# Kernel optimization log

Hardware: AMD Instinct MI355X
Metric: run time of the kernel (lower is better)

The kernel has to match this reference:

```python
import jax, jax.numpy as jnp
import numpy as np

NUM_EMBEDDINGS = 8192
EMBED_DIM = 256
BETA = 0.25  # commitment loss weight (self.beta in the torch module)


def setup_inputs() -> dict:
    key = jax.random.key(0)
    k1, k2 = jax.random.split(key)
    z = jax.random.normal(k1, (16, EMBED_DIM, 32, 32), dtype=jnp.float32)
    # learned codebook (nn.Embedding weight), default init ~ N(0,1); scale for realism
    codebook = jax.random.normal(k2, (NUM_EMBEDDINGS, EMBED_DIM), dtype=jnp.float32)
    return {"z": z, "codebook": codebook}


def reference(z, codebook):
    # channel_last: [B, C, H, W] -> [B, H, W, C]
    zl = jnp.transpose(z, (0, 2, 3, 1))
    # d = ||e||^2 - 2 z.e  (the ||z||^2 term is constant w.r.t. argmin, as in source)
    d = jnp.sum(codebook * codebook, axis=1) - 2.0 * jnp.einsum('bhwd,nd->bhwn', zl, codebook)
    index = jnp.argmin(d, axis=-1)          # [B, H, W] int
    z_q = codebook[index]                   # [B, H, W, C]
    loss = (jnp.mean((jax.lax.stop_gradient(z_q) - zl) ** 2)
            + BETA * jnp.mean((z_q - jax.lax.stop_gradient(zl)) ** 2))
    # straight-through estimator
    z_q_st = zl + jax.lax.stop_gradient(z_q - zl)
    # diversity: mean over batch of (#unique codes used per sample) / (#positions per sample)
    B = index.shape[0]
    flat = index.reshape(B, -1)             # [B, HW]
    presence = jnp.zeros((B, NUM_EMBEDDINGS), jnp.float32).at[
        jnp.arange(B)[:, None], flat].set(1.0)
    diversity = presence.sum() / jnp.float32(flat.size)
    # channel_first: [B, H, W, C] -> [B, C, H, W]
    z_q_out = jnp.transpose(z_q_st, (0, 3, 1, 2))
    return z_q_out, index, loss, diversity
```

## Files before the change

### kernel.cpp

```cpp
#include <hip/hip_runtime.h>
#include <cstdint>

typedef unsigned short u16;
typedef unsigned int   u32;
typedef __attribute__((ext_vector_type(8))) short bf16x8;
typedef __attribute__((ext_vector_type(4))) float f32x4;

#define NPOS    16384
#define DIM     256
#define NCODES  8192
#define ZSTRIDE 262144
#define NELEM   4194304
#define TAU     6e-3f
#define RCH     32


#define WS_AHI    0u
#define WS_ALO    8388608u
#define WS_BHI    16777216u
#define WS_BLO    20971520u
#define WS_E2     25165824u
#define WS_WV1    25198592u
#define WS_WI1    27295744u
#define WS_WV2    29392896u
#define WS_IDX    31490048u
#define WS_PRES   31555584u
#define WS_RCNT   31571968u
#define WS_LDEL   31571972u
#define WS_RLIST  31572224u
#define WS_PART   31637760u
#define WS_RBV    31638784u
#define WS_RBI    33735936u

__device__ __forceinline__ u16 f2bf(float x) {
    u32 u = __float_as_uint(x);
    return (u16)((u + 0x7FFFu + ((u >> 16) & 1u)) >> 16);
}
__device__ __forceinline__ float bf2f(u16 h) { return __uint_as_float((u32)h << 16); }

__device__ __forceinline__ void gload_lds16(const void* g, void* l) {
    __builtin_amdgcn_global_load_lds(
        (const __attribute__((address_space(1))) void*)g,
        (__attribute__((address_space(3))) void*)l, 16, 0, 0);
}

__device__ __forceinline__ void top2_push(float& v1, int& i1, float& v2, float d, int c) {
    const bool better = d < v1;
    v2 = fminf(v2, fmaxf(d, v1));
    v1 = fminf(v1, d);
    if (better) i1 = c;
}
__device__ __forceinline__ void top2_merge(float& v1, int& i1, float& v2,
                                           float ov1, int oi1, float ov2) {
    const bool better = ov1 < v1;
    v2 = fminf(fminf(v2, ov2), fmaxf(v1, ov1));
    v1 = fminf(v1, ov1);
    if (better) i1 = oi1;
}

__global__ __launch_bounds__(256)
void preprocess(const float* __restrict__ cb, const float* __restrict__ z,
                u16* __restrict__ Bhi, u16* __restrict__ Blo,
                u16* __restrict__ Ahi, u16* __restrict__ Alo,
                float* __restrict__ e2, u32* __restrict__ presence,
                int* __restrict__ rcnt, float* __restrict__ ldel) {
    __shared__ u16 his[128 * 34], los[128 * 34];
    const int bid = blockIdx.x;
    const int t   = threadIdx.x;

    if (bid < 2048) {
        if (bid < 16) presence[bid * 256 + t] = 0u;
        if (bid == 16 && t == 0) { rcnt[0] = 0; ldel[0] = 0.0f; }

        const int row  = bid * 4 + (t >> 6);
        const int lane = t & 63;
        const float4 v = *(const float4*)(cb + (size_t)row * DIM + lane * 4);
        float s = v.x * v.x + v.y * v.y + v.z * v.z + v.w * v.w;
#pragma unroll
        for (int o = 32; o > 0; o >>= 1) s += __shfl_xor(s, o);
        if (lane == 0) e2[row] = s;

        const float vv[4] = {v.x, v.y, v.z, v.w};
        u16 h[4], l[4];
#pragma unroll
        for (int j = 0; j < 4; ++j) { h[j] = f2bf(vv[j]); l[j] = f2bf(vv[j] - bf2f(h[j])); }

        const int nt = row >> 8, pr = row & 255, kt = lane >> 3;
        const int q  = (lane & 7) >> 1, off = (lane & 1) * 4;
        const int sw = (pr >> 1) & 3;
        const size_t dst = ((size_t)(nt * 8 + kt) * 256 + pr) * 32 + ((q ^ sw) << 3) + off;
        *(uint2*)(Bhi + dst) = make_uint2((u32)h[0] | ((u32)h[1] << 16), (u32)h[2] | ((u32)h[3] << 16));
        *(uint2*)(Blo + dst) = make_uint2((u32)l[0] | ((u32)l[1] << 16), (u32)l[2] | ((u32)l[3] << 16));
        return;
    }

    const int zb = bid - 2048;
    const int m128 = zb >> 3, kt = zb & 7;
    const int mtb = m128 >> 1, prb = (m128 & 1) * 128;
    const int b = m128 >> 3, hw0 = (m128 & 7) * 128;
    const int p = t & 127, ch = t >> 7;

#pragma unroll
    for (int sub = 0; sub < 16; ++sub) {
        const int cl = sub * 2 + ch;
        const float v = z[(size_t)b * ZSTRIDE + (size_t)(kt * 32 + cl) * 1024 + hw0 + p];
        const u16 h = f2bf(v);
        his[p * 34 + cl] = h;
        los[p * 34 + cl] = f2bf(v - bf2f(h));
    }
    __syncthreads();
    const int p2 = t >> 1, c0 = (t & 1) * 2;
    const int sw = (p2 >> 1) & 3;
    const size_t base = ((size_t)(mtb * 8 + kt) * 256 + prb + p2) * 32;
    u32 wh[8], wl[8];
    const int half = c0 * 8;
#pragma unroll
    for (int j = 0; j < 8; ++j) {
        wh[j] = (u32)his[p2 * 34 + half + 2 * j] | ((u32)his[p2 * 34 + half + 2 * j + 1] << 16);
        wl[j] = (u32)los[p2 * 34 + half + 2 * j] | ((u32)los[p2 * 34 + half + 2 * j + 1] << 16);
    }
    *(uint4*)(Ahi + base + (((c0 + 0) ^ sw) << 3)) = make_uint4(wh[0], wh[1], wh[2], wh[3]);
    *(uint4*)(Ahi + base + (((c0 + 1) ^ sw) << 3)) = make_uint4(wh[4], wh[5], wh[6], wh[7]);
    *(uint4*)(Alo + base + (((c0 + 0) ^ sw) << 3)) = make_uint4(wl[0], wl[1], wl[2], wl[3]);
    *(uint4*)(Alo + base + (((c0 + 1) ^ sw) << 3)) = make_uint4(wl[4], wl[5], wl[6], wl[7]);
}

__global__ __launch_bounds__(512, 2)
void gemm256(const u16* __restrict__ Ahi, const u16* __restrict__ Alo,
             const u16* __restrict__ Bhi, const u16* __restrict__ Blo,
             const float* __restrict__ e2,
             float* __restrict__ wv1, int* __restrict__ wi1, float* __restrict__ wv2) {
    __shared__ u16 sbuf[2][4][8192];
    __shared__ __align__(16) float e2s[1024];
    __shared__ float lv1[1024]; __shared__ int li1[1024]; __shared__ float lv2[1024];

    const int bid = blockIdx.x;
    const int ng  = bid & 7;
    const int mtb = bid >> 3;

    const int tid  = threadIdx.x;
    const int lane = tid & 63;
    const int wave = tid >> 6;
    const int wr   = wave >> 2, wc = wave & 3;
    const int l15  = lane & 15, lq = lane >> 4;
    const int woff = wave * 1024;
    const int src  = tid * 8;
    const int sel  = (l15 >> 1) & 3;
    const int ka   = ((lq ^ sel) << 3);

#define FRAG(base, row) (*(const bf16x8*)((base) + (row) * 32 + ka))
#define STAGE(bq, ss_) do {                                                     \
        const int ntl_ = (ss_) >> 3, kt_ = (ss_) & 7;                           \
        const int nt_  = ng * 4 + ntl_;                                         \
        const u16* Ah_ = Ahi + (size_t)(mtb * 8 + kt_) * 8192;                  \
        const u16* Al_ = Alo + (size_t)(mtb * 8 + kt_) * 8192;                  \
        const u16* Bh_ = Bhi + (size_t)(nt_ * 8 + kt_) * 8192;                  \
        const u16* Bl_ = Blo + (size_t)(nt_ * 8 + kt_) * 8192;                  \
        gload_lds16(Ah_ + src,        (char*)&sbuf[bq][0][0] + woff);           \
        gload_lds16(Ah_ + 4096 + src, (char*)&sbuf[bq][0][0] + 8192 + woff);    \
        gload_lds16(Al_ + src,        (char*)&sbuf[bq][1][0] + woff);           \
        gload_lds16(Al_ + 4096 + src, (char*)&sbuf[bq][1][0] + 8192 + woff);    \
        gload_lds16(Bh_ + src,        (char*)&sbuf[bq][2][0] + woff);           \
        gload_lds16(Bh_ + 4096 + src, (char*)&sbuf[bq][2][0] + 8192 + woff);    \
        gload_lds16(Bl_ + src,        (char*)&sbuf[bq][3][0] + woff);           \
        gload_lds16(Bl_ + 4096 + src, (char*)&sbuf[bq][3][0] + 8192 + woff);    \
    } while (0)

    f32x4 acc[8][4] = {};
    float e2v[4];
    int cbase = 0;

    e2s[tid]       = e2[ng * 1024 + tid];
    e2s[tid + 512] = e2[ng * 1024 + 512 + tid];
    __syncthreads();
    STAGE(0, 0);
    __syncthreads();

    for (int ss = 0; ss < 32; ++ss) {
        const int cur = ss & 1;
        if (ss < 31) STAGE(cur ^ 1, ss + 1);

        if ((ss & 7) == 0) {
            const int ntl = ss >> 3;
            cbase = (ng * 4 + ntl) * 256 + wc * 64 + l15;
            const int eb = ntl * 256 + wc * 64 + l15;
#pragma unroll
            for (int ni = 0; ni < 4; ++ni) e2v[ni] = e2s[eb + ni * 16];
        }

        const u16* Ah = &sbuf[cur][0][0];
        const u16* Al = &sbuf[cur][1][0];
        const u16* Bh = &sbuf[cur][2][0];
        const u16* Bl = &sbuf[cur][3][0];

        bf16x8 ah[8], bh[4], xx[8];
#pragma unroll
        for (int i = 0; i < 8; ++i) ah[i] = FRAG(Ah, wr * 128 + i * 16 + l15);
#pragma unroll
        for (int i = 0; i < 4; ++i) bh[i] = FRAG(Bh, wc * 64 + i * 16 + l15);
#pragma unroll
        for (int i = 0; i < 8; ++i)
#pragma unroll
            for (int j = 0; j < 4; ++j)
                acc[i][j] = __builtin_amdgcn_mfma_f32_16x16x32_bf16(ah[i], bh[j], acc[i][j], 0, 0, 0);
#pragma unroll
        for (int j = 0; j < 4; ++j) xx[j] = FRAG(Bl, wc * 64 + j * 16 + l15);
#pragma unroll
        for (int i = 0; i < 8; ++i)
#pragma unroll
            for (int j = 0; j < 4; ++j)
                acc[i][j] = __builtin_amdgcn_mfma_f32_16x16x32_bf16(ah[i], xx[j], acc[i][j], 0, 0, 0);
#pragma unroll
        for (int i = 0; i < 8; ++i) xx[i] = FRAG(Al, wr * 128 + i * 16 + l15);
#pragma unroll
        for (int i = 0; i < 8; ++i)
#pragma unroll
            for (int j = 0; j < 4; ++j)
                acc[i][j] = __builtin_amdgcn_mfma_f32_16x16x32_bf16(xx[i], bh[j], acc[i][j], 0, 0, 0);

        if ((ss & 7) == 7) {
            const int ntl = ss >> 3;
#pragma unroll
            for (int mi = 0; mi < 8; ++mi)
#pragma unroll
                for (int j = 0; j < 4; ++j) {
                    float v1 = 3e38f, v2 = 3e38f; int i1 = 0;
#pragma unroll
                    for (int ni = 0; ni < 4; ++ni) {
                        const float d = fmaf(-2.0f, acc[mi][ni][j], e2v[ni]);
                        top2_push(v1, i1, v2, d, cbase + ni * 16);
                    }
#pragma unroll
                    for (int off = 1; off <= 8; off <<= 1) {
                        const float ov1 = __shfl_xor(v1, off);
                        const int   oi1 = __shfl_xor(i1, off);
                        const float ov2 = __shfl_xor(v2, off);
                        top2_merge(v1, i1, v2, ov1, oi1, ov2);
                    }
                    if (l15 == 0) {
                        const int row = wr * 128 + mi * 16 + lq * 4 + j;
                        lv1[row * 4 + wc] = v1; li1[row * 4 + wc] = i1; lv2[row * 4 + wc] = v2;
                    }
                }
            __syncthreads();
            if (tid < 256) {
                float v1 = lv1[tid * 4], v2 = lv2[tid * 4]; int i1 = li1[tid * 4];
#pragma unroll
                for (int g = 1; g < 4; ++g)
                    top2_merge(v1, i1, v2, lv1[tid * 4 + g], li1[tid * 4 + g], lv2[tid * 4 + g]);
                const size_t o = (size_t)(ng * 4 + ntl) * NPOS + (size_t)mtb * 256 + tid;
                wv1[o] = v1; wi1[o] = i1; wv2[o] = v2;
            }
#pragma unroll
            for (int mi = 0; mi < 8; ++mi)
#pragma unroll
                for (int ni = 0; ni < 4; ++ni)
                    acc[mi][ni] = f32x4{0.f, 0.f, 0.f, 0.f};
        }
        __syncthreads();
    }
#undef FRAG
#undef STAGE
}

__global__ __launch_bounds__(256)
void merge_output(const float* __restrict__ wv1, const int* __restrict__ wi1,
                  const float* __restrict__ wv2,
                  const float* __restrict__ z, const float* __restrict__ cb,
                  float* __restrict__ out, float* __restrict__ out_idxf,
                  float* __restrict__ partial, u32* __restrict__ presence,
                  int* __restrict__ rcnt, int* __restrict__ rlist,
                  int* __restrict__ ws_idx) {
    __shared__ int codes[64];
    __shared__ float red[256];
    const int tile = blockIdx.x;
    const int b    = tile >> 4;
    const int hw0  = (tile & 15) * 64;
    const int tid  = threadIdx.x;
    const int m    = tid & 63;
    const int cg   = tid >> 6;

    if (cg == 0) {
        const int pos = tile * 64 + m;
        float v1 = 3e38f, v2 = 3e38f; int i1 = 0;
#pragma unroll
        for (int g = 0; g < 32; ++g) {
            const size_t o = (size_t)g * NPOS + pos;
            top2_merge(v1, i1, v2, wv1[o], wi1[o], wv2[o]);
        }
        codes[m]      = i1;
        ws_idx[pos]   = i1;
        out_idxf[pos] = (float)i1;
        if (v2 - v1 < TAU) {
            const int s = atomicAdd(rcnt, 1);
            rlist[s] = pos;
        } else {
            atomicOr(&presence[b * 256 + (i1 >> 5)], 1u << (i1 & 31));
        }
    }
    __syncthreads();

    const int code = codes[m];
    const float* crow = cb  + (size_t)code * DIM;
    const float* zb   = z   + (size_t)b * ZSTRIDE + hw0 + m;
    float*       ob   = out + (size_t)b * ZSTRIDE + hw0 + m;

    float lsum = 0.0f;
#pragma unroll
    for (int q = 0; q < 16; ++q) {
        const int c = (cg * 16 + q) * 4;
        const float4 e = *(const float4*)(crow + c);
        const float z0 = zb[(size_t)(c + 0) * 1024];
        const float z1 = zb[(size_t)(c + 1) * 1024];
        const float z2 = zb[(size_t)(c + 2) * 1024];
        const float z3 = zb[(size_t)(c + 3) * 1024];
        const float d0 = e.x - z0, d1 = e.y - z1, d2 = e.z - z2, d3 = e.w - z3;
        lsum += d0 * d0 + d1 * d1 + d2 * d2 + d3 * d3;
        ob[(size_t)(c + 0) * 1024] = z0 + d0;
        ob[(size_t)(c + 1) * 1024] = z1 + d1;
        ob[(size_t)(c + 2) * 1024] = z2 + d2;
        ob[(size_t)(c + 3) * 1024] = z3 + d3;
    }
    red[tid] = lsum;
    __syncthreads();
    for (int o = 128; o > 0; o >>= 1) {
        if (tid < o) red[tid] += red[tid + o];
        __syncthreads();
    }
    if (tid == 0) partial[tile] = red[0];
}

__global__ __launch_bounds__(256)
void rescue_scan(const float* __restrict__ z, const float* __restrict__ cb,
                 const float* __restrict__ e2, const int* __restrict__ rcnt,
                 const int* __restrict__ rlist,
                 float* __restrict__ rbv, int* __restrict__ rbi) {
    __shared__ float zvec[256];
    const int n = rcnt[0];
    const int t = threadIdx.x;
    const int w = t >> 6, l = t & 63;
    const int njobs = n * 8;
    for (int idx = blockIdx.x; idx < njobs; idx += gridDim.x) {
        const int e  = idx >> 3;
        const int cg = idx & 7;
        const int pos = rlist[e];
        const int b = pos >> 10, hw = pos & 1023;
        __syncthreads();
        zvec[t] = z[(size_t)b * ZSTRIDE + (size_t)t * 1024 + hw];
        __syncthreads();

        const int ch = cg * 4 + w;
        const int c0 = ch * 256 + l * 4;
        float bv = 3e38f; int bi = 0x7fffffff;
#pragma unroll
        for (int j = 0; j < 4; ++j) {
            const int c = c0 + j;
            const float* cr = cb + (size_t)c * DIM;
            float a0 = 0.f, a1 = 0.f, a2 = 0.f, a3 = 0.f;
#pragma unroll
            for (int k = 0; k < DIM; k += 16) {
                const float4 v0 = *(const float4*)(cr + k);
                const float4 v1 = *(const float4*)(cr + k + 4);
                const float4 v2 = *(const float4*)(cr + k + 8);
                const float4 v3 = *(const float4*)(cr + k + 12);
                a0 = fmaf(zvec[k + 0], v0.x, a0); a0 = fmaf(zvec[k + 1], v0.y, a0);
                a0 = fmaf(zvec[k + 2], v0.z, a0); a0 = fmaf(zvec[k + 3], v0.w, a0);
                a1 = fmaf(zvec[k + 4], v1.x, a1); a1 = fmaf(zvec[k + 5], v1.y, a1);
                a1 = fmaf(zvec[k + 6], v1.z, a1); a1 = fmaf(zvec[k + 7], v1.w, a1);
                a2 = fmaf(zvec[k + 8], v2.x, a2); a2 = fmaf(zvec[k + 9], v2.y, a2);
                a2 = fmaf(zvec[k +10], v2.z, a2); a2 = fmaf(zvec[k +11], v2.w, a2);
                a3 = fmaf(zvec[k +12], v3.x, a3); a3 = fmaf(zvec[k +13], v3.y, a3);
                a3 = fmaf(zvec[k +14], v3.z, a3); a3 = fmaf(zvec[k +15], v3.w, a3);
            }
            const float dot = (a0 + a1) + (a2 + a3);
            const float d = fmaf(-2.f, dot, e2[c]);
            if (d < bv) { bv = d; bi = c; }
        }
#pragma unroll
        for (int off = 1; off <= 32; off <<= 1) {
            const float ov = __shfl_xor(bv, off);
            const int   oi = __shfl_xor(bi, off);
            if (ov < bv || (ov == bv && oi < bi)) { bv = ov; bi = oi; }
        }
        if (l == 0) { rbv[e * RCH + ch] = bv; rbi[e * RCH + ch] = bi; }
    }
}

__global__ __launch_bounds__(256)
void rescue_fix(const float* __restrict__ z, const float* __restrict__ cb,
                const int* __restrict__ rcnt, const int* __restrict__ rlist,
                const float* __restrict__ rbv, const int* __restrict__ rbi,
                const int* __restrict__ ws_idx,
                float* __restrict__ out_idxf, u32* __restrict__ presence,
                float* __restrict__ out, float* __restrict__ ldel) {
    __shared__ int   bestc_sh;
    __shared__ float red[4];
    const int n = rcnt[0];
    const int t = threadIdx.x;
    for (int e = blockIdx.x; e < n; e += gridDim.x) {
        const int pos = rlist[e];
        const int b = pos >> 10, hw = pos & 1023;
        if (t < 64) {
            float v = 3e38f; int i = 0x7fffffff;
            if (t < 32) { v = rbv[e * RCH + t]; i = rbi[e * RCH + t]; }
#pragma unroll
            for (int off = 1; off <= 32; off <<= 1) {
                const float ov = __shfl_xor(v, off);
                const int   oi = __shfl_xor(i, off);
                if (ov < v || (ov == v && oi < i)) { v = ov; i = oi; }
            }
            if (t == 0) {
                bestc_sh = i;
                out_idxf[pos] = (float)i;
                atomicOr(&presence[b * 256 + (i >> 5)], 1u << (i & 31));
            }
        }
        __syncthreads();
        const int best = bestc_sh;
        const int old  = ws_idx[pos];
        if (best != old) {
            const float zv = z[(size_t)b * ZSTRIDE + (size_t)t * 1024 + hw];
            const float en = cb[(size_t)best * DIM + t];
            const float eo = cb[(size_t)old  * DIM + t];
            const float dn = en - zv, dold = eo - zv;
            out[(size_t)b * ZSTRIDE + (size_t)t * 1024 + hw] = zv + dn;
            float dl = dn * dn - dold * dold;
#pragma unroll
            for (int o = 32; o > 0; o >>= 1) dl += __shfl_xor(dl, o);
            if ((t & 63) == 0) red[t >> 6] = dl;
            __syncthreads();
            if (t == 0) atomicAdd(ldel, red[0] + red[1] + red[2] + red[3]);
        }
        __syncthreads();
    }
}

__global__ __launch_bounds__(256)
void finalize_kernel(const float* __restrict__ partial,
                     const u32* __restrict__ presence,
                     const float* __restrict__ ldel,
                     float* __restrict__ out_loss, float* __restrict__ out_div) {
    __shared__ float sred[256];
    __shared__ int   ired[256];
    const int tid = threadIdx.x;
    float s = partial[tid];
    int cnt = 0;
    for (int w = tid; w < 16 * 256; w += 256) cnt += __popc(presence[w]);
    sred[tid] = s; ired[tid] = cnt;
    __syncthreads();
    for (int o = 128; o > 0; o >>= 1) {
        if (tid < o) { sred[tid] += sred[tid + o]; ired[tid] += ired[tid + o]; }
        __syncthreads();
    }
    if (tid == 0) {
        out_loss[0] = 1.25f * (sred[0] + ldel[0]) / (float)NELEM;
        out_div[0]  = (float)ired[0] / (float)NPOS;
    }
}

extern "C" void kernel_launch(void* const* d_in, const int* in_sizes, int n_in,
                              void* d_out, int out_size, void* d_ws, size_t ws_size,
                              hipStream_t stream) {
    const float* z  = (const float*)d_in[0];
    const float* cb = (const float*)d_in[1];
    float* out = (float*)d_out;
    char*  ws  = (char*)d_ws;

    u16*   Ahi = (u16*)(ws + WS_AHI);
    u16*   Alo = (u16*)(ws + WS_ALO);
    u16*   Bhi = (u16*)(ws + WS_BHI);
    u16*   Blo = (u16*)(ws + WS_BLO);
    float* e2  = (float*)(ws + WS_E2);
    float* wv1 = (float*)(ws + WS_WV1);
    int*   wi1 = (int*)(ws + WS_WI1);
    float* wv2 = (float*)(ws + WS_WV2);
    int*   ws_idx = (int*)(ws + WS_IDX);
    u32*   presence = (u32*)(ws + WS_PRES);
    int*   rcnt  = (int*)(ws + WS_RCNT);
    float* ldel  = (float*)(ws + WS_LDEL);
    int*   rlist = (int*)(ws + WS_RLIST);
    float* partial = (float*)(ws + WS_PART);
    float* rbv = (float*)(ws + WS_RBV);
    int*   rbi = (int*)(ws + WS_RBI);

    float* out_zq   = out;
    float* out_idxf = out + NELEM;
    float* out_loss = out + NELEM + NPOS;
    float* out_div  = out + NELEM + NPOS + 1;

    preprocess<<<3072, 256, 0, stream>>>(cb, z, Bhi, Blo, Ahi, Alo, e2, presence, rcnt, ldel);
    gemm256<<<512, 512, 0, stream>>>(Ahi, Alo, Bhi, Blo, e2, wv1, wi1, wv2);
    merge_output<<<NPOS / 64, 256, 0, stream>>>(wv1, wi1, wv2, z, cb, out_zq, out_idxf,
                                                partial, presence, rcnt, rlist, ws_idx);
    rescue_scan<<<2048, 256, 0, stream>>>(z, cb, e2, rcnt, rlist, rbv, rbi);
    rescue_fix<<<512, 256, 0, stream>>>(z, cb, rcnt, rlist, rbv, rbi, ws_idx,
                                        out_idxf, presence, out_zq, ldel);
    finalize_kernel<<<1, 256, 0, stream>>>(partial, presence, ldel, out_loss, out_div);
}
```

Before: 298.3 us.

## Interleave per-matrix prefetch with MFMA phases using fine-grained waitcnt and setprio

```diff
diff --git a/kernel.cpp b/kernel.cpp
--- a/kernel.cpp
+++ b/kernel.cpp
@@ -149,22 +149,18 @@
     const int ka   = ((lq ^ sel) << 3);
 
 #define FRAG(base, row) (*(const bf16x8*)((base) + (row) * 32 + ka))
-#define STAGE(bq, ss_) do {                                                     \
-        const int ntl_ = (ss_) >> 3, kt_ = (ss_) & 7;                           \
-        const int nt_  = ng * 4 + ntl_;                                         \
-        const u16* Ah_ = Ahi + (size_t)(mtb * 8 + kt_) * 8192;                  \
-        const u16* Al_ = Alo + (size_t)(mtb * 8 + kt_) * 8192;                  \
-        const u16* Bh_ = Bhi + (size_t)(nt_ * 8 + kt_) * 8192;                  \
-        const u16* Bl_ = Blo + (size_t)(nt_ * 8 + kt_) * 8192;                  \
-        gload_lds16(Ah_ + src,        (char*)&sbuf[bq][0][0] + woff);           \
-        gload_lds16(Ah_ + 4096 + src, (char*)&sbuf[bq][0][0] + 8192 + woff);    \
-        gload_lds16(Al_ + src,        (char*)&sbuf[bq][1][0] + woff);           \
-        gload_lds16(Al_ + 4096 + src, (char*)&sbuf[bq][1][0] + 8192 + woff);    \
-        gload_lds16(Bh_ + src,        (char*)&sbuf[bq][2][0] + woff);           \
-        gload_lds16(Bh_ + 4096 + src, (char*)&sbuf[bq][2][0] + 8192 + woff);    \
-        gload_lds16(Bl_ + src,        (char*)&sbuf[bq][3][0] + woff);           \
-        gload_lds16(Bl_ + 4096 + src, (char*)&sbuf[bq][3][0] + 8192 + woff);    \
+#define STG(bq, ss_, m) do {                                                     \
+        const int ntl_ = (ss_) >> 3, kt_ = (ss_) & 7;                             \
+        const int nt_  = ng * 4 + ntl_;                                           \
+        const u16* P_ = ((m) == 0 ? Ahi : (m) == 1 ? Alo : (m) == 2 ? Bhi : Blo)  \
+            + (size_t)((((m) < 2) ? (mtb * 8 + kt_) : (nt_ * 8 + kt_))) * 8192;   \
+        gload_lds16(P_ + src,        (char*)&sbuf[bq][m][0] + woff);              \
+        gload_lds16(P_ + 4096 + src, (char*)&sbuf[bq][m][0] + 8192 + woff);       \
     } while (0)
+#define BAR()   __builtin_amdgcn_s_barrier()
+#define LGKM0() do { asm volatile("s_waitcnt lgkmcnt(0)" ::: "memory");           \
+                     __builtin_amdgcn_sched_barrier(0); } while (0)
+#define VM(N)   asm volatile("s_waitcnt vmcnt(" #N ")" ::: "memory")
 
     f32x4 acc[8][4] = {};
     float e2v[4];
@@ -173,12 +169,14 @@
     e2s[tid]       = e2[ng * 1024 + tid];
     e2s[tid + 512] = e2[ng * 1024 + 512 + tid];
     __syncthreads();
-    STAGE(0, 0);
-    __syncthreads();
+    STG(0, 0, 0); STG(0, 0, 2); STG(0, 0, 3); STG(0, 0, 1);
+    VM(4);
+    BAR();
 
     for (int ss = 0; ss < 32; ++ss) {
         const int cur = ss & 1;
-        if (ss < 31) STAGE(cur ^ 1, ss + 1);
+        const int nxt = cur ^ 1;
+        const bool pf = ss < 31;
 
         if ((ss & 7) == 0) {
             const int ntl = ss >> 3;
@@ -193,30 +191,83 @@
         const u16* Bh = &sbuf[cur][2][0];
         const u16* Bl = &sbuf[cur][3][0];
 
-        bf16x8 ah[8], bh[4], xx[8];
-#pragma unroll
-        for (int i = 0; i < 8; ++i) ah[i] = FRAG(Ah, wr * 128 + i * 16 + l15);
-#pragma unroll
-        for (int i = 0; i < 4; ++i) bh[i] = FRAG(Bh, wc * 64 + i * 16 + l15);
-#pragma unroll
-        for (int i = 0; i < 8; ++i)
+        bf16x8 ah[8], bh[4], bl[4], al[8];
+
+#pragma unroll
+        for (int i = 0; i < 4; ++i) ah[i] = FRAG(Ah, wr * 128 + i * 16 + l15);
+#pragma unroll
+        for (int j = 0; j < 4; ++j) bh[j] = FRAG(Bh, wc * 64 + j * 16 + l15);
+        if (pf) STG(nxt, ss + 1, 0);
+        BAR(); LGKM0();
+        __builtin_amdgcn_s_setprio(1);
+#pragma unroll
+        for (int i = 0; i < 4; ++i)
 #pragma unroll
             for (int j = 0; j < 4; ++j)
                 acc[i][j] = __builtin_amdgcn_mfma_f32_16x16x32_bf16(ah[i], bh[j], acc[i][j], 0, 0, 0);
-#pragma unroll
-        for (int j = 0; j < 4; ++j) xx[j] = FRAG(Bl, wc * 64 + j * 16 + l15);
-#pragma unroll
-        for (int i = 0; i < 8; ++i)
+        __builtin_amdgcn_s_setprio(0);
+        BAR();
+
+#pragma unroll
+        for (int i = 4; i < 8; ++i) ah[i] = FRAG(Ah, wr * 128 + i * 16 + l15);
+        if (pf) STG(nxt, ss + 1, 2);
+        BAR(); LGKM0();
+        __builtin_amdgcn_s_setprio(1);
+#pragma unroll
+        for (int i = 4; i < 8; ++i)
 #pragma unroll
             for (int j = 0; j < 4; ++j)
-                acc[i][j] = __builtin_amdgcn_mfma_f32_16x16x32_bf16(ah[i], xx[j], acc[i][j], 0, 0, 0);
-#pragma unroll
-        for (int i = 0; i < 8; ++i) xx[i] = FRAG(Al, wr * 128 + i * 16 + l15);
-#pragma unroll
-        for (int i = 0; i < 8; ++i)
+                acc[i][j] = __builtin_amdgcn_mfma_f32_16x16x32_bf16(ah[i], bh[j], acc[i][j], 0, 0, 0);
+        __builtin_amdgcn_s_setprio(0);
+        if (pf) { VM(4); } else { VM(0); }
+        BAR();
+
+#pragma unroll
+        for (int j = 0; j < 4; ++j) bl[j] = FRAG(Bl, wc * 64 + j * 16 + l15);
+        if (pf) STG(nxt, ss + 1, 3);
+        BAR(); LGKM0();
+        __builtin_amdgcn_s_setprio(1);
+#pragma unroll
+        for (int i = 0; i < 4; ++i)
 #pragma unroll
             for (int j = 0; j < 4; ++j)
-                acc[i][j] = __builtin_amdgcn_mfma_f32_16x16x32_bf16(xx[i], bh[j], acc[i][j], 0, 0, 0);
+                acc[i][j] = __builtin_amdgcn_mfma_f32_16x16x32_bf16(ah[i], bl[j], acc[i][j], 0, 0, 0);
+        __builtin_amdgcn_s_setprio(0);
+        BAR();
+
+        if (pf) STG(nxt, ss + 1, 1);
+        BAR();
+        __builtin_amdgcn_s_setprio(1);
+#pragma unroll
+        for (int i = 4; i < 8; ++i)
+#pragma unroll
+            for (int j = 0; j < 4; ++j)
+                acc[i][j] = __builtin_amdgcn_mfma_f32_16x16x32_bf16(ah[i], bl[j], acc[i][j], 0, 0, 0);
+        __builtin_amdgcn_s_setprio(0);
+        BAR();
+
+#pragma unroll
+        for (int i = 0; i < 4; ++i) al[i] = FRAG(Al, wr * 128 + i * 16 + l15);
+        BAR(); LGKM0();
+        __builtin_amdgcn_s_setprio(1);
+#pragma unroll
+        for (int i = 0; i < 4; ++i)
+#pragma unroll
+            for (int j = 0; j < 4; ++j)
+                acc[i][j] = __builtin_amdgcn_mfma_f32_16x16x32_bf16(al[i], bh[j], acc[i][j], 0, 0, 0);
+        __builtin_amdgcn_s_setprio(0);
+        BAR();
+
+#pragma unroll
+        for (int i = 4; i < 8; ++i) al[i] = FRAG(Al, wr * 128 + i * 16 + l15);
+        BAR(); LGKM0();
+        __builtin_amdgcn_s_setprio(1);
+#pragma unroll
+        for (int i = 4; i < 8; ++i)
+#pragma unroll
+            for (int j = 0; j < 4; ++j)
+                acc[i][j] = __builtin_amdgcn_mfma_f32_16x16x32_bf16(al[i], bh[j], acc[i][j], 0, 0, 0);
+        __builtin_amdgcn_s_setprio(0);
 
         if ((ss & 7) == 7) {
             const int ntl = ss >> 3;
@@ -257,10 +308,15 @@
                 for (int ni = 0; ni < 4; ++ni)
                     acc[mi][ni] = f32x4{0.f, 0.f, 0.f, 0.f};
         }
-        __syncthreads();
+
+        if (pf) { VM(4); } else { VM(0); }
+        BAR();
     }
 #undef FRAG
-#undef STAGE
+#undef STG
+#undef BAR
+#undef LGKM0
+#undef VM
 }
 
 __global__ __launch_bounds__(256)
```

New measurement: 309.5 us. 3.7% more time.
